# Optimization experiments

Measured on AMD Instinct MI355X. Metric: run time of the kernel, lower is better.

Reference implementation:

```python
import jax, jax.numpy as jnp
import numpy as np

S, E, C = 8192, 64, 256  # tokens, experts, capacity


def setup_inputs() -> dict:
    key = jax.random.key(0)
    k1, k2, k3, k4 = jax.random.split(key, 4)
    logits = jax.random.normal(k1, (S, E), dtype=jnp.float32)
    # top-2 expert assignment (mask2 is the second choice, disjoint from mask1)
    top1 = jnp.argmax(logits, axis=1)
    mask1 = jax.nn.one_hot(top1, E, dtype=jnp.float32)
    masked = logits - mask1 * 1e9
    top2 = jnp.argmax(masked, axis=1)
    mask2 = jax.nn.one_hot(top2, E, dtype=jnp.float32)
    # one-hot capacity slot encodings [s, c]
    loc1 = jax.nn.one_hot(jax.random.randint(k3, (S,), 0, C), C, dtype=jnp.float32)
    loc2 = jax.nn.one_hot(jax.random.randint(k4, (S,), 0, C), C, dtype=jnp.float32)
    return {
        "logits": logits,
        "mask1_float": mask1,
        "mask2_float": mask2,
        "locations1_sc": loc1,
        "locations2_sc": loc2,
    }


def reference(logits, mask1_float, mask2_float, locations1_sc, locations2_sc):
    gates = jax.nn.softmax(logits, axis=1)                      # [s, e]
    num_experts = gates.shape[1]
    me = jnp.mean(gates, axis=0)                                # [e]
    ce = jnp.mean(mask1_float, axis=0)                          # [e]
    l_aux = jnp.mean(me * ce) * num_experts * num_experts
    gates1_s = jnp.einsum('se,se->s', gates, mask1_float)       # [s]
    gates2_s = jnp.einsum('se,se->s', gates, mask2_float)       # [s]
    denom_s = gates1_s + gates2_s
    denom_s = jnp.maximum(denom_s, jnp.finfo(denom_s.dtype).eps)
    gates1_s = gates1_s / denom_s
    gates2_s = gates2_s / denom_s
    gates1 = gates1_s[:, None] * mask1_float                    # [s, e]
    gates2 = gates2_s[:, None] * mask2_float                    # [s, e]
    combine1_sec = jnp.einsum('se,sc->sec', gates1, locations1_sc)
    combine2_sec = jnp.einsum('se,sc->sec', gates2, locations2_sc)
    combine_weights = combine1_sec + combine2_sec               # [s, e, c]
    return (l_aux, combine_weights)
```

## Files before the change

### kernel.cpp

```cpp
#include <hip/hip_runtime.h>
#include <hip/hip_bf16.h>
#include <float.h>

constexpr int S = 8192;
constexpr int E = 64;
constexpr int C = 256;
constexpr int K1_BLOCKS = 256;
constexpr int ROWS_PER_BLOCK = S / K1_BLOCKS;

__global__ void zero_kernel(float4* __restrict__ out4, size_t n4, float* __restrict__ out_tail) {
    size_t i = (size_t)blockIdx.x * blockDim.x + threadIdx.x;
    size_t stride = (size_t)gridDim.x * blockDim.x;
    const float4 z = make_float4(0.f, 0.f, 0.f, 0.f);
    for (; i < n4; i += stride) out4[i] = z;
    if (blockIdx.x == 0 && threadIdx.x == 0) *out_tail = 0.f;
}

__global__ __launch_bounds__(256) void compute_kernel(
        const float* __restrict__ logits,
        const float* __restrict__ mask1,
        const float* __restrict__ mask2,
        const float* __restrict__ loc1,
        const float* __restrict__ loc2,
        float* __restrict__ out,
        float* __restrict__ ws_partials) {
    __shared__ float me_s[4][64];
    __shared__ float ce_s[4][64];

    const int lane = threadIdx.x & 63;
    const int wave = threadIdx.x >> 6;
    const int row0 = blockIdx.x * ROWS_PER_BLOCK;

    float me_acc = 0.f;
    float ce_acc = 0.f;

    for (int r = wave; r < ROWS_PER_BLOCK; r += 4) {
        const int s = row0 + r;
        float x = logits[(size_t)s * E + lane];
        float mx = x;
        #pragma unroll
        for (int off = 32; off > 0; off >>= 1) mx = fmaxf(mx, __shfl_xor(mx, off));
        float ex = __expf(x - mx);
        float sum = ex;
        #pragma unroll
        for (int off = 32; off > 0; off >>= 1) sum += __shfl_xor(sum, off);
        const float g = ex / sum;

        const float m1v = mask1[(size_t)s * E + lane];
        const float m2v = mask2[(size_t)s * E + lane];
        me_acc += g;
        ce_acc += m1v;

        float g1 = g * m1v, g2 = g * m2v;
        float e1f = m1v * (float)lane, e2f = m2v * (float)lane;
        #pragma unroll
        for (int off = 32; off > 0; off >>= 1) {
            g1  += __shfl_xor(g1,  off);
            g2  += __shfl_xor(g2,  off);
            e1f += __shfl_xor(e1f, off);
            e2f += __shfl_xor(e2f, off);
        }

        const float4 l1v = *reinterpret_cast<const float4*>(loc1 + (size_t)s * C + lane * 4);
        const float4 l2v = *reinterpret_cast<const float4*>(loc2 + (size_t)s * C + lane * 4);
        float c1f = 0.f, c2f = 0.f;
        const float base_idx = (float)(lane * 4);
        if (l1v.x > 0.5f) c1f = base_idx + 0.f;
        if (l1v.y > 0.5f) c1f = base_idx + 1.f;
        if (l1v.z > 0.5f) c1f = base_idx + 2.f;
        if (l1v.w > 0.5f) c1f = base_idx + 3.f;
        if (l2v.x > 0.5f) c2f = base_idx + 0.f;
        if (l2v.y > 0.5f) c2f = base_idx + 1.f;
        if (l2v.z > 0.5f) c2f = base_idx + 2.f;
        if (l2v.w > 0.5f) c2f = base_idx + 3.f;
        #pragma unroll
        for (int off = 32; off > 0; off >>= 1) {
            c1f = fmaxf(c1f, __shfl_xor(c1f, off));
            c2f = fmaxf(c2f, __shfl_xor(c2f, off));
        }

        if (lane == 0) {
            float denom = g1 + g2;
            denom = fmaxf(denom, FLT_EPSILON);
            const float w1 = g1 / denom;
            const float w2 = g2 / denom;
            const int e1 = (int)(e1f + 0.5f);
            const int e2 = (int)(e2f + 0.5f);
            const int c1 = (int)(c1f + 0.5f);
            const int c2 = (int)(c2f + 0.5f);
            const size_t base = 1 + (size_t)s * (E * C);
            out[base + (size_t)e1 * C + c1] = w1;
            out[base + (size_t)e2 * C + c2] = w2;
        }
    }

    me_s[wave][lane] = me_acc;
    ce_s[wave][lane] = ce_acc;
    __syncthreads();
    if (threadIdx.x < 64) {
        const float me_b = me_s[0][lane] + me_s[1][lane] + me_s[2][lane] + me_s[3][lane];
        const float ce_b = ce_s[0][lane] + ce_s[1][lane] + ce_s[2][lane] + ce_s[3][lane];
        ws_partials[(size_t)blockIdx.x * 128 + lane]      = me_b;
        ws_partials[(size_t)blockIdx.x * 128 + 64 + lane] = ce_b;
    }
}

__global__ void laux_kernel(const float* __restrict__ ws_partials, float* __restrict__ out) {
    const int lane = threadIdx.x;
    float me = 0.f, ce = 0.f;
    for (int b = 0; b < K1_BLOCKS; ++b) {
        me += ws_partials[(size_t)b * 128 + lane];
        ce += ws_partials[(size_t)b * 128 + 64 + lane];
    }
    float prod = me * ce;
    #pragma unroll
    for (int off = 32; off > 0; off >>= 1) prod += __shfl_xor(prod, off);
    if (lane == 0) {
        out[0] = prod * (float)E / ((float)S * (float)S);
    }
}

extern "C" void kernel_launch(void* const* d_in, const int* in_sizes, int n_in,
                              void* d_out, int out_size, void* d_ws, size_t ws_size,
                              hipStream_t stream) {
    const float* logits = (const float*)d_in[0];
    const float* mask1  = (const float*)d_in[1];
    const float* mask2  = (const float*)d_in[2];
    const float* loc1   = (const float*)d_in[3];
    const float* loc2   = (const float*)d_in[4];
    float* out = (float*)d_out;
    float* ws  = (float*)d_ws;

    const size_t n4 = (size_t)(out_size - 1) / 4;
    zero_kernel<<<2048, 256, 0, stream>>>((float4*)out, n4, out + (size_t)out_size - 1);

    compute_kernel<<<K1_BLOCKS, 256, 0, stream>>>(logits, mask1, mask2, loc1, loc2, out, ws);

    laux_kernel<<<1, 64, 0, stream>>>(ws, out);
}
```

Measured before the change: 143.1 us.

## Use hipMemsetAsync for zeroing, ballot-based index finding, more blocks

Replaces the custom zero-fill kernel with hipMemsetAsync on the large output. Finds the expert and slot indices with wave ballots and ffs instead of butterfly shuffle reductions. Doubles the compute grid to 512 blocks with contiguous rows per wave, and parallelises the final l_aux reduction across four waves. The aim is to cut the shuffle work and the reduction latency, while relying on the runtime memset for the bandwidth-bound fill.

```diff
diff --git a/kernel.cpp b/kernel.cpp
--- a/kernel.cpp
+++ b/kernel.cpp
@@ -5,16 +5,8 @@
 constexpr int S = 8192;
 constexpr int E = 64;
 constexpr int C = 256;
-constexpr int K1_BLOCKS = 256;
-constexpr int ROWS_PER_BLOCK = S / K1_BLOCKS;
-
-__global__ void zero_kernel(float4* __restrict__ out4, size_t n4, float* __restrict__ out_tail) {
-    size_t i = (size_t)blockIdx.x * blockDim.x + threadIdx.x;
-    size_t stride = (size_t)gridDim.x * blockDim.x;
-    const float4 z = make_float4(0.f, 0.f, 0.f, 0.f);
-    for (; i < n4; i += stride) out4[i] = z;
-    if (blockIdx.x == 0 && threadIdx.x == 0) *out_tail = 0.f;
-}
+constexpr int A_BLOCKS = 512;
+constexpr int ROWS_PER_WAVE = S / (A_BLOCKS * 4);
 
 __global__ __launch_bounds__(256) void compute_kernel(
         const float* __restrict__ logits,
@@ -29,18 +21,19 @@
 
     const int lane = threadIdx.x & 63;
     const int wave = threadIdx.x >> 6;
-    const int row0 = blockIdx.x * ROWS_PER_BLOCK;
 
     float me_acc = 0.f;
     float ce_acc = 0.f;
 
-    for (int r = wave; r < ROWS_PER_BLOCK; r += 4) {
-        const int s = row0 + r;
-        float x = logits[(size_t)s * E + lane];
+    #pragma unroll
+    for (int r = 0; r < ROWS_PER_WAVE; ++r) {
+        const int s = blockIdx.x * (4 * ROWS_PER_WAVE) + wave * ROWS_PER_WAVE + r;
+
+        const float x = logits[(size_t)s * E + lane];
         float mx = x;
         #pragma unroll
         for (int off = 32; off > 0; off >>= 1) mx = fmaxf(mx, __shfl_xor(mx, off));
-        float ex = __expf(x - mx);
+        const float ex = __expf(x - mx);
         float sum = ex;
         #pragma unroll
         for (int off = 32; off > 0; off >>= 1) sum += __shfl_xor(sum, off);
@@ -51,46 +44,31 @@
         me_acc += g;
         ce_acc += m1v;
 
-        float g1 = g * m1v, g2 = g * m2v;
-        float e1f = m1v * (float)lane, e2f = m2v * (float)lane;
-        #pragma unroll
-        for (int off = 32; off > 0; off >>= 1) {
-            g1  += __shfl_xor(g1,  off);
-            g2  += __shfl_xor(g2,  off);
-            e1f += __shfl_xor(e1f, off);
-            e2f += __shfl_xor(e2f, off);
-        }
+        const unsigned long long b1 = __ballot(m1v > 0.5f);
+        const unsigned long long b2 = __ballot(m2v > 0.5f);
+        const int e1 = __ffsll(b1) - 1;
+        const int e2 = __ffsll(b2) - 1;
+        const float g1 = __shfl(g, e1);
+        const float g2 = __shfl(g, e2);
 
         const float4 l1v = *reinterpret_cast<const float4*>(loc1 + (size_t)s * C + lane * 4);
         const float4 l2v = *reinterpret_cast<const float4*>(loc2 + (size_t)s * C + lane * 4);
-        float c1f = 0.f, c2f = 0.f;
-        const float base_idx = (float)(lane * 4);
-        if (l1v.x > 0.5f) c1f = base_idx + 0.f;
-        if (l1v.y > 0.5f) c1f = base_idx + 1.f;
-        if (l1v.z > 0.5f) c1f = base_idx + 2.f;
-        if (l1v.w > 0.5f) c1f = base_idx + 3.f;
-        if (l2v.x > 0.5f) c2f = base_idx + 0.f;
-        if (l2v.y > 0.5f) c2f = base_idx + 1.f;
-        if (l2v.z > 0.5f) c2f = base_idx + 2.f;
-        if (l2v.w > 0.5f) c2f = base_idx + 3.f;
-        #pragma unroll
-        for (int off = 32; off > 0; off >>= 1) {
-            c1f = fmaxf(c1f, __shfl_xor(c1f, off));
-            c2f = fmaxf(c2f, __shfl_xor(c2f, off));
-        }
+        const int bm1 = (l1v.x > 0.5f ? 1 : 0) | (l1v.y > 0.5f ? 2 : 0) |
+                        (l1v.z > 0.5f ? 4 : 0) | (l1v.w > 0.5f ? 8 : 0);
+        const int bm2 = (l2v.x > 0.5f ? 1 : 0) | (l2v.y > 0.5f ? 2 : 0) |
+                        (l2v.z > 0.5f ? 4 : 0) | (l2v.w > 0.5f ? 8 : 0);
+        const int L1 = __ffsll(__ballot(bm1 != 0)) - 1;
+        const int L2 = __ffsll(__ballot(bm2 != 0)) - 1;
+        const int sub1 = __ffs(__shfl(bm1, L1)) - 1;
+        const int sub2 = __ffs(__shfl(bm2, L2)) - 1;
 
         if (lane == 0) {
-            float denom = g1 + g2;
-            denom = fmaxf(denom, FLT_EPSILON);
-            const float w1 = g1 / denom;
-            const float w2 = g2 / denom;
-            const int e1 = (int)(e1f + 0.5f);
-            const int e2 = (int)(e2f + 0.5f);
-            const int c1 = (int)(c1f + 0.5f);
-            const int c2 = (int)(c2f + 0.5f);
+            const int c1 = L1 * 4 + sub1;
+            const int c2 = L2 * 4 + sub2;
+            const float denom = fmaxf(g1 + g2, FLT_EPSILON);
             const size_t base = 1 + (size_t)s * (E * C);
-            out[base + (size_t)e1 * C + c1] = w1;
-            out[base + (size_t)e2 * C + c2] = w2;
+            out[base + (size_t)e1 * C + c1] = g1 / denom;
+            out[base + (size_t)e2 * C + c2] = g2 / denom;
         }
     }
 
@@ -105,18 +83,27 @@
     }
 }
 
-__global__ void laux_kernel(const float* __restrict__ ws_partials, float* __restrict__ out) {
-    const int lane = threadIdx.x;
+__global__ __launch_bounds__(256) void laux_kernel(const float* __restrict__ ws_partials,
+                                                   float* __restrict__ out) {
+    __shared__ float mes[4][64];
+    __shared__ float ces[4][64];
+    const int e = threadIdx.x & 63;
+    const int q = threadIdx.x >> 6;
     float me = 0.f, ce = 0.f;
-    for (int b = 0; b < K1_BLOCKS; ++b) {
-        me += ws_partials[(size_t)b * 128 + lane];
-        ce += ws_partials[(size_t)b * 128 + 64 + lane];
+    for (int b = q; b < A_BLOCKS; b += 4) {
+        me += ws_partials[(size_t)b * 128 + e];
+        ce += ws_partials[(size_t)b * 128 + 64 + e];
     }
-    float prod = me * ce;
-    #pragma unroll
-    for (int off = 32; off > 0; off >>= 1) prod += __shfl_xor(prod, off);
-    if (lane == 0) {
-        out[0] = prod * (float)E / ((float)S * (float)S);
+    mes[q][e] = me;
+    ces[q][e] = ce;
+    __syncthreads();
+    if (threadIdx.x < 64) {
+        const float m = mes[0][e] + mes[1][e] + mes[2][e] + mes[3][e];
+        const float c = ces[0][e] + ces[1][e] + ces[2][e] + ces[3][e];
+        float prod = m * c;
+        #pragma unroll
+        for (int off = 32; off > 0; off >>= 1) prod += __shfl_xor(prod, off);
+        if (e == 0) out[0] = prod * (float)E / ((float)S * (float)S);
     }
 }
 
@@ -131,10 +118,9 @@
     float* out = (float*)d_out;
     float* ws  = (float*)d_ws;
 
-    const size_t n4 = (size_t)(out_size - 1) / 4;
-    zero_kernel<<<2048, 256, 0, stream>>>((float4*)out, n4, out + (size_t)out_size - 1);
+    hipMemsetAsync(out, 0, (size_t)out_size * sizeof(float), stream);
 
-    compute_kernel<<<K1_BLOCKS, 256, 0, stream>>>(logits, mask1, mask2, loc1, loc2, out, ws);
+    compute_kernel<<<A_BLOCKS, 256, 0, stream>>>(logits, mask1, mask2, loc1, loc2, out, ws);
 
-    laux_kernel<<<1, 64, 0, stream>>>(ws, out);
+    laux_kernel<<<1, 256, 0, stream>>>(ws, out);
 }
```

Result: faster. 131.1 us (-8.4%).
